# Kernel optimization log

Hardware: AMD Instinct MI355X
Metric: run time of the kernel (lower is better)

Reference implementation:

```python
import jax, jax.numpy as jnp
import numpy as np

N = 50000      # nodes
E = 400000     # edges
IN = 128       # in_dim == emb_dim (residual requires equality)
POS = 64       # pos_in_dim
EMB = 128
LN_EPS = 1e-5


def _ln(x, g, b):
    m = jnp.mean(x, axis=-1, keepdims=True)
    v = jnp.mean((x - m) ** 2, axis=-1, keepdims=True)
    return (x - m) / jnp.sqrt(v + LN_EPS) * g + b


def _gin(x, src, dst, eps, W1, b1, g1, be1, W2, b2):
    # GINConv: mlp((1+eps)*x + sum_{j in N(i)} x_j)
    agg = jax.ops.segment_sum(x[src], dst, num_segments=x.shape[0])
    h = (1.0 + eps) * x + agg
    h = jax.nn.relu(_ln(h @ W1 + b1, g1, be1))
    return h @ W2 + b2


def setup_inputs() -> dict:
    key = jax.random.key(0)
    ks = jax.random.split(key, 8)
    x = jax.random.normal(ks[0], (N, IN), jnp.float32)
    pos = jax.random.normal(ks[1], (N, POS), jnp.float32)
    edge_index = jax.random.randint(ks[2], (2, E), 0, N)
    d = IN + POS
    f32 = jnp.float32
    W1 = (jax.random.normal(ks[3], (d, EMB), f32) / np.sqrt(d))
    W2 = (jax.random.normal(ks[4], (EMB, EMB), f32) / np.sqrt(EMB))
    W1p = (jax.random.normal(ks[5], (POS, EMB), f32) / np.sqrt(POS))
    W2p = (jax.random.normal(ks[6], (EMB, EMB), f32) / np.sqrt(EMB))
    z = jnp.zeros((EMB,), f32)
    o = jnp.ones((EMB,), f32)
    return {
        "x": x, "pos": pos, "edge_index": edge_index,
        "eps": jnp.zeros((), f32), "W1": W1, "b1": z, "g1": o, "be1": z,
        "W2": W2, "b2": z, "ln_g": o, "ln_b": z,
        "epsp": jnp.zeros((), f32), "W1p": W1p, "b1p": z, "g1p": o, "be1p": z,
        "W2p": W2p, "b2p": z, "lnp_g": o, "lnp_b": z,
    }


def reference(x, pos, edge_index, eps, W1, b1, g1, be1, W2, b2, ln_g, ln_b,
              epsp, W1p, b1p, g1p, be1p, W2p, b2p, lnp_g, lnp_b):
    src, dst = edge_index[0], edge_index[1]
    node_feats = jnp.concatenate([x, pos], axis=-1)  # [N, IN+POS]
    h = jax.nn.relu(_ln(_gin(node_feats, src, dst, eps, W1, b1, g1, be1, W2, b2), ln_g, ln_b))
    p = jax.nn.relu(_ln(_gin(pos, src, dst, epsp, W1p, b1p, g1p, be1p, W2p, b2p), lnp_g, lnp_b))
    # dropout is identity in eval mode (model_drop_ratio applied only when training)
    h = h + x  # add_residual=True
    return (h, p)
```

## Files before the change

kernel.cpp:

```cpp
#include <hip/hip_runtime.h>

#define NN    50000
#define NPAD  50048
#define HB    391
#define EE    400000
#define IND   128
#define POSD  64
#define DD    192
#define EMBD  128
#define LNEPS 1e-5f
#define CAP   32

#define PREP_B 4692
#define FILL_B 1563
#define WC_B   256

typedef __attribute__((ext_vector_type(8))) short bf16x8;
typedef __attribute__((ext_vector_type(4))) unsigned short u16x4;
typedef __attribute__((ext_vector_type(4))) float f32x4;
typedef unsigned short ushort_t;
typedef unsigned int uint_t;

#define MFMA16 __builtin_amdgcn_mfma_f32_16x16x32_bf16

__device__ inline ushort_t f2bf(float f) {
  union { float f; unsigned u; } v; v.f = f;
  unsigned r = (v.u + 0x7FFFu + ((v.u >> 16) & 1u)) >> 16;
  return (ushort_t)r;
}
__device__ inline float bf2f(unsigned u) {
  union { unsigned u; float f; } v; v.u = u << 16;
  return v.f;
}

__global__ __launch_bounds__(256) void prep_k(
    const float* __restrict__ x, const float* __restrict__ pos,
    const int* __restrict__ ei,
    const float* __restrict__ W1, const float* __restrict__ W2,
    const float* __restrict__ W1p, const float* __restrict__ W2p,
    int* __restrict__ cnt, int* __restrict__ csr,
    ushort_t* __restrict__ cat, ushort_t* __restrict__ wt) {
  const int bid = blockIdx.x;
  if (bid < PREP_B) {
    int id  = bid * 256 + threadIdx.x;
    int n   = id / 24, sub = id - n * 24;
    bf16x8 o = (bf16x8){0, 0, 0, 0, 0, 0, 0, 0};
    if (n < NN) {
      const float* src = (sub < 16) ? (x + (size_t)n * IND + sub * 8)
                                    : (pos + (size_t)n * POSD + (sub - 16) * 8);
      f32x4 v0 = *(const f32x4*)(src);
      f32x4 v1 = *(const f32x4*)(src + 4);
#pragma unroll
      for (int i = 0; i < 4; ++i) {
        o[i]     = (short)f2bf(v0[i]);
        o[i + 4] = (short)f2bf(v1[i]);
      }
    }
    *(bf16x8*)(cat + (size_t)n * DD + sub * 8) = o;
  } else if (bid < PREP_B + FILL_B) {
    int e = (bid - PREP_B) * 256 + threadIdx.x;
    if (e < EE) {
      int src = ei[e];
      int dst = ei[EE + e];
      int idx = atomicAdd(&cnt[dst], 1);
      if (idx < CAP) csr[(size_t)dst * CAP + idx] = src;
    }
  } else {
    int t = (bid - PREP_B - FILL_B) * 256 + threadIdx.x;
    if (t < 24576) {
      int c = t / 192, k = t % 192;
      wt[t] = f2bf(W1[k * EMBD + c]);
    } else if (t < 40960) {
      int q = t - 24576; int c = q / 128, k = q % 128;
      wt[t] = f2bf(W2[k * EMBD + c]);
    } else if (t < 49152) {
      int q = t - 40960; int c = q / 64, k = q % 64;
      wt[t] = f2bf(W1p[k * EMBD + c]);
    } else {
      int q = t - 49152; int c = q / 128, k = q % 128;
      wt[t] = f2bf(W2p[k * EMBD + c]);
    }
  }
}

__global__ __launch_bounds__(256) void fill_k(
    const int* __restrict__ ei, int* __restrict__ cnt, int* __restrict__ csr) {
  int e = blockIdx.x * 256 + threadIdx.x;
  if (e >= EE) return;
  int src = ei[e];
  int dst = ei[EE + e];
  int idx = atomicAdd(&cnt[dst], 1);
  if (idx < CAP) csr[(size_t)dst * CAP + idx] = src;
}

__global__ __launch_bounds__(256) void wconv_k(
    const float* __restrict__ W1, const float* __restrict__ W2,
    const float* __restrict__ W1p, const float* __restrict__ W2p,
    ushort_t* __restrict__ wt) {
  int tid = blockIdx.x * 256 + threadIdx.x;
  if (tid < 24576) {
    int c = tid / 192, k = tid % 192;
    wt[tid] = f2bf(W1[k * EMBD + c]);
  } else if (tid < 40960) {
    int t = tid - 24576; int c = t / 128, k = t % 128;
    wt[tid] = f2bf(W2[k * EMBD + c]);
  } else if (tid < 49152) {
    int t = tid - 40960; int c = t / 64, k = t % 64;
    wt[tid] = f2bf(W1p[k * EMBD + c]);
  } else {
    int t = tid - 49152; int c = t / 128, k = t % 128;
    wt[tid] = f2bf(W2p[k * EMBD + c]);
  }
}

__global__ __launch_bounds__(256) void gather_k(
    const float* __restrict__ x, const float* __restrict__ pos,
    const int* __restrict__ cnt, const int* __restrict__ csr,
    const float* __restrict__ epsv, const float* __restrict__ epspv,
    ushort_t* __restrict__ h0, ushort_t* __restrict__ p0) {
  const int lane = threadIdx.x & 63;
  const int wv   = threadIdx.x >> 6;
  const int n    = blockIdx.x * 4 + wv;
  if (n >= NPAD) return;

  float a0 = 0.f, a1 = 0.f, a2 = 0.f;
  float xs0 = 0.f, xs1 = 0.f, ps = 0.f;

  if (n < NN) {
    int deg = cnt[n]; if (deg > CAP) deg = CAP;
    const int* row = csr + (size_t)n * CAP;
    int idx = (lane < deg) ? row[lane] : 0;
    int t = 0;
    for (; t + 2 <= deg; t += 2) {
      int s1 = __shfl(idx, t);
      int s2 = __shfl(idx, t + 1);
      float u0 = x[(size_t)s1 * IND + lane];
      float u1 = x[(size_t)s1 * IND + 64 + lane];
      float u2 = pos[(size_t)s1 * POSD + lane];
      float v0 = x[(size_t)s2 * IND + lane];
      float v1 = x[(size_t)s2 * IND + 64 + lane];
      float v2 = pos[(size_t)s2 * POSD + lane];
      a0 += u0 + v0; a1 += u1 + v1; a2 += u2 + v2;
    }
    if (t < deg) {
      int s1 = __shfl(idx, t);
      a0 += x[(size_t)s1 * IND + lane];
      a1 += x[(size_t)s1 * IND + 64 + lane];
      a2 += pos[(size_t)s1 * POSD + lane];
    }
    xs0 = x[(size_t)n * IND + lane];
    xs1 = x[(size_t)n * IND + 64 + lane];
    ps  = pos[(size_t)n * POSD + lane];
  }

  float e1  = 1.0f + epsv[0];
  float ep1 = 1.0f + epspv[0];
  h0[(size_t)n * DD + lane]       = f2bf(fmaf(e1, xs0, a0));
  h0[(size_t)n * DD + 64 + lane]  = f2bf(fmaf(e1, xs1, a1));
  h0[(size_t)n * DD + 128 + lane] = f2bf(fmaf(e1, ps,  a2));
  p0[(size_t)n * POSD + lane]     = f2bf(fmaf(ep1, ps, a2));
}

__global__ __launch_bounds__(256) void gather2_k(
    const ushort_t* __restrict__ cat, const int* __restrict__ cnt,
    const int* __restrict__ csr,
    const float* __restrict__ epsv, const float* __restrict__ epspv,
    ushort_t* __restrict__ h0, ushort_t* __restrict__ p0) {
  const int lane = threadIdx.x & 63;
  const int wv   = threadIdx.x >> 6;
  const int half = lane >> 5;
  const int l2   = lane & 31;
  const int n    = blockIdx.x * 8 + wv * 2 + half;

  int deg = 0;
  if (n < NN) { deg = cnt[n]; if (deg > CAP) deg = CAP; }
  int idx = (l2 < deg) ? csr[(size_t)n * CAP + l2] : 0;

  float a0 = 0.f, a1 = 0.f, a2 = 0.f, a3 = 0.f, a4 = 0.f, a5 = 0.f;
  int t = 0;
  for (; t + 2 <= deg; t += 2) {
    int s1 = __shfl(idx, half * 32 + t);
    int s2 = __shfl(idx, half * 32 + t + 1);
    const ushort_t* r1 = cat + (size_t)s1 * DD;
    const ushort_t* r2 = cat + (size_t)s2 * DD;
    u16x4 u1 = *(const u16x4*)(r1 + l2 * 4);
    uint_t v1 = *(const uint_t*)(r1 + 128 + l2 * 2);
    u16x4 u2 = *(const u16x4*)(r2 + l2 * 4);
    uint_t v2 = *(const uint_t*)(r2 + 128 + l2 * 2);
    a0 += bf2f(u1[0]) + bf2f(u2[0]);
    a1 += bf2f(u1[1]) + bf2f(u2[1]);
    a2 += bf2f(u1[2]) + bf2f(u2[2]);
    a3 += bf2f(u1[3]) + bf2f(u2[3]);
    a4 += bf2f(v1 & 0xffffu) + bf2f(v2 & 0xffffu);
    a5 += bf2f(v1 >> 16) + bf2f(v2 >> 16);
  }
  if (t < deg) {
    int s1 = __shfl(idx, half * 32 + t);
    const ushort_t* r1 = cat + (size_t)s1 * DD;
    u16x4 u1 = *(const u16x4*)(r1 + l2 * 4);
    uint_t v1 = *(const uint_t*)(r1 + 128 + l2 * 2);
    a0 += bf2f(u1[0]); a1 += bf2f(u1[1]);
    a2 += bf2f(u1[2]); a3 += bf2f(u1[3]);
    a4 += bf2f(v1 & 0xffffu); a5 += bf2f(v1 >> 16);
  }

  const float e1  = 1.0f + epsv[0];
  const float ep1 = 1.0f + epspv[0];
  const ushort_t* self = cat + (size_t)n * DD;
  u16x4 su = *(const u16x4*)(self + l2 * 4);
  uint_t sv = *(const uint_t*)(self + 128 + l2 * 2);

  u16x4 o;
  o[0] = f2bf(fmaf(e1, bf2f(su[0]), a0));
  o[1] = f2bf(fmaf(e1, bf2f(su[1]), a1));
  o[2] = f2bf(fmaf(e1, bf2f(su[2]), a2));
  o[3] = f2bf(fmaf(e1, bf2f(su[3]), a3));
  *(u16x4*)(h0 + (size_t)n * DD + l2 * 4) = o;

  float p4 = bf2f(sv & 0xffffu), p5 = bf2f(sv >> 16);
  uint_t oh = (uint_t)f2bf(fmaf(e1, p4, a4)) |
              ((uint_t)f2bf(fmaf(e1, p5, a5)) << 16);
  *(uint_t*)(h0 + (size_t)n * DD + 128 + l2 * 2) = oh;
  uint_t op = (uint_t)f2bf(fmaf(ep1, p4, a4)) |
              ((uint_t)f2bf(fmaf(ep1, p5, a5)) << 16);
  *(uint_t*)(p0 + (size_t)n * POSD + l2 * 2) = op;
}

__device__ inline void ln_epi(f32x4 (&acc)[2][8],
                              const float* __restrict__ bias,
                              const float* __restrict__ gam,
                              const float* __restrict__ bet, int c0) {
  float bv[8], gv[8], bev[8];
#pragma unroll
  for (int nt = 0; nt < 8; ++nt) {
    bv[nt]  = bias[nt * 16 + c0];
    gv[nt]  = gam[nt * 16 + c0];
    bev[nt] = bet[nt * 16 + c0];
  }
#pragma unroll
  for (int mt = 0; mt < 2; ++mt) {
#pragma unroll
    for (int r = 0; r < 4; ++r) {
      float s = 0.f, sq = 0.f;
#pragma unroll
      for (int nt = 0; nt < 8; ++nt) {
        float v = acc[mt][nt][r] + bv[nt];
        acc[mt][nt][r] = v;
        s += v; sq += v * v;
      }
#pragma unroll
      for (int off = 1; off < 16; off <<= 1) {
        s  += __shfl_xor(s, off);
        sq += __shfl_xor(sq, off);
      }
      float mean = s * (1.0f / 128.0f);
      float var  = sq * (1.0f / 128.0f) - mean * mean;
      float rstd = rsqrtf(var + LNEPS);
#pragma unroll
      for (int nt = 0; nt < 8; ++nt) {
        acc[mt][nt][r] =
            fmaxf(fmaf((acc[mt][nt][r] - mean) * rstd, gv[nt], bev[nt]), 0.f);
      }
    }
  }
}

__device__ inline void act_write(char* act, f32x4 (&acc)[2][8], int g, int c0) {
#pragma unroll
  for (int mt = 0; mt < 2; ++mt)
#pragma unroll
    for (int nt = 0; nt < 8; ++nt)
#pragma unroll
      for (int r = 0; r < 4; ++r) {
        int lr   = mt * 16 + g * 4 + r;
        int byte = lr * 256 + (((nt * 16 + c0) * 2) ^ ((lr & 7) << 4));
        *(ushort_t*)(act + byte) = f2bf(acc[mt][nt][r]);
      }
}

__device__ inline void stage_w(const ushort_t* __restrict__ src, char* dst,
                               int rowbytes, int chunks, int tid) {
  int cpr = rowbytes >> 4;
  for (int i = tid; i < chunks; i += 256) {
    int row  = i / cpr;
    int colb = (i - row * cpr) << 4;
    *(bf16x8*)(dst + row * rowbytes + (colb ^ ((row & 7) << 4))) =
        *(const bf16x8*)(src + (size_t)i * 8);
  }
}

__global__ __launch_bounds__(256) void mlp_k(
    const ushort_t* __restrict__ h0, const ushort_t* __restrict__ p0,
    const ushort_t* __restrict__ wt,
    const float* __restrict__ b1, const float* __restrict__ g1,
    const float* __restrict__ be1,
    const float* __restrict__ b2, const float* __restrict__ lng,
    const float* __restrict__ lnb,
    const float* __restrict__ b1p, const float* __restrict__ g1p,
    const float* __restrict__ be1p,
    const float* __restrict__ b2p, const float* __restrict__ lnpg,
    const float* __restrict__ lnpb,
    const float* __restrict__ x, float* __restrict__ out) {
  __shared__ __align__(16) char smem[81920];
  const int tid  = threadIdx.x;
  const int lane = tid & 63;
  const int wv   = tid >> 6;
  const int g    = lane >> 4;
  const int c0   = lane & 15;
  const int bid  = blockIdx.x;
  char* act = smem + 49152 + wv * 8192;

  f32x4 acc[2][8];

  if (bid < HB) {
    const int m0 = bid * 128;
    stage_w(wt, smem, 384, 3072, tid);
    bf16x8 a0[6], a1[6];
    const size_t r0 = (size_t)(m0 + wv * 32 + c0) * DD;
    const size_t r1 = r0 + (size_t)16 * DD;
#pragma unroll
    for (int ks = 0; ks < 6; ++ks) {
      a0[ks] = *(const bf16x8*)(h0 + r0 + ks * 32 + g * 8);
      a1[ks] = *(const bf16x8*)(h0 + r1 + ks * 32 + g * 8);
    }
    __syncthreads();

#pragma unroll
    for (int mt = 0; mt < 2; ++mt)
#pragma unroll
      for (int nt = 0; nt < 8; ++nt) acc[mt][nt] = (f32x4){0.f, 0.f, 0.f, 0.f};
#pragma unroll
    for (int ks = 0; ks < 6; ++ks)
#pragma unroll
      for (int nt = 0; nt < 8; ++nt) {
        int wrow = nt * 16 + c0;
        bf16x8 b = *(const bf16x8*)(smem + wrow * 384 +
                                    ((ks * 64 + g * 16) ^ ((wrow & 7) << 4)));
        acc[0][nt] = MFMA16(a0[ks], b, acc[0][nt], 0, 0, 0);
        acc[1][nt] = MFMA16(a1[ks], b, acc[1][nt], 0, 0, 0);
      }
    ln_epi(acc, b1, g1, be1, c0);
    act_write(act, acc, g, c0);
    __syncthreads();
    stage_w(wt + 24576, smem, 256, 2048, tid);
    __syncthreads();

#pragma unroll
    for (int mt = 0; mt < 2; ++mt)
#pragma unroll
      for (int nt = 0; nt < 8; ++nt) acc[mt][nt] = (f32x4){0.f, 0.f, 0.f, 0.f};
#pragma unroll
    for (int ks = 0; ks < 4; ++ks) {
      bf16x8 am[2];
#pragma unroll
      for (int mt = 0; mt < 2; ++mt) {
        int lr = mt * 16 + c0;
        am[mt] = *(const bf16x8*)(act + lr * 256 +
                                  (((ks * 32 + g * 8) * 2) ^ ((lr & 7) << 4)));
      }
#pragma unroll
      for (int nt = 0; nt < 8; ++nt) {
        int wrow = nt * 16 + c0;
        bf16x8 b = *(const bf16x8*)(smem + wrow * 256 +
                                    ((ks * 64 + g * 16) ^ ((wrow & 7) << 4)));
        acc[0][nt] = MFMA16(am[0], b, acc[0][nt], 0, 0, 0);
        acc[1][nt] = MFMA16(am[1], b, acc[1][nt], 0, 0, 0);
      }
    }
    ln_epi(acc, b2, lng, lnb, c0);
#pragma unroll
    for (int mt = 0; mt < 2; ++mt)
#pragma unroll
      for (int nt = 0; nt < 8; ++nt)
#pragma unroll
        for (int r = 0; r < 4; ++r) {
          int node = m0 + wv * 32 + mt * 16 + g * 4 + r;
          int col  = nt * 16 + c0;
          if (node < NN)
            out[(size_t)node * EMBD + col] =
                acc[mt][nt][r] + x[(size_t)node * IND + col];
        }
  } else {
    const int m0 = (bid - HB) * 128;
    stage_w(wt + 40960, smem, 128, 1024, tid);
    stage_w(wt + 49152, smem + 16384, 256, 2048, tid);
    bf16x8 a0[2], a1[2];
    const size_t r0 = (size_t)(m0 + wv * 32 + c0) * POSD;
    const size_t r1 = r0 + (size_t)16 * POSD;
#pragma unroll
    for (int ks = 0; ks < 2; ++ks) {
      a0[ks] = *(const bf16x8*)(p0 + r0 + ks * 32 + g * 8);
      a1[ks] = *(const bf16x8*)(p0 + r1 + ks * 32 + g * 8);
    }
    __syncthreads();

#pragma unroll
    for (int mt = 0; mt < 2; ++mt)
#pragma unroll
      for (int nt = 0; nt < 8; ++nt) acc[mt][nt] = (f32x4){0.f, 0.f, 0.f, 0.f};
#pragma unroll
    for (int ks = 0; ks < 2; ++ks)
#pragma unroll
      for (int nt = 0; nt < 8; ++nt) {
        int wrow = nt * 16 + c0;
        bf16x8 b = *(const bf16x8*)(smem + wrow * 128 +
                                    ((ks * 64 + g * 16) ^ ((wrow & 7) << 4)));
        acc[0][nt] = MFMA16(a0[ks], b, acc[0][nt], 0, 0, 0);
        acc[1][nt] = MFMA16(a1[ks], b, acc[1][nt], 0, 0, 0);
      }
    ln_epi(acc, b1p, g1p, be1p, c0);
    act_write(act, acc, g, c0);

#pragma unroll
    for (int mt = 0; mt < 2; ++mt)
#pragma unroll
      for (int nt = 0; nt < 8; ++nt) acc[mt][nt] = (f32x4){0.f, 0.f, 0.f, 0.f};
#pragma unroll
    for (int ks = 0; ks < 4; ++ks) {
      bf16x8 am[2];
#pragma unroll
      for (int mt = 0; mt < 2; ++mt) {
        int lr = mt * 16 + c0;
        am[mt] = *(const bf16x8*)(act + lr * 256 +
                                  (((ks * 32 + g * 8) * 2) ^ ((lr & 7) << 4)));
      }
#pragma unroll
      for (int nt = 0; nt < 8; ++nt) {
        int wrow = nt * 16 + c0;
        bf16x8 b = *(const bf16x8*)(smem + 16384 + wrow * 256 +
                                    ((ks * 64 + g * 16) ^ ((wrow & 7) << 4)));
        acc[0][nt] = MFMA16(am[0], b, acc[0][nt], 0, 0, 0);
        acc[1][nt] = MFMA16(am[1], b, acc[1][nt], 0, 0, 0);
      }
    }
    ln_epi(acc, b2p, lnpg, lnpb, c0);
#pragma unroll
    for (int mt = 0; mt < 2; ++mt)
#pragma unroll
      for (int nt = 0; nt < 8; ++nt)
#pragma unroll
        for (int r = 0; r < 4; ++r) {
          int node = m0 + wv * 32 + mt * 16 + g * 4 + r;
          int col  = nt * 16 + c0;
          if (node < NN)
            out[(size_t)NN * EMBD + (size_t)node * EMBD + col] = acc[mt][nt][r];
        }
  }
}

extern "C" void kernel_launch(void* const* d_in, const int* in_sizes, int n_in,
                              void* d_out, int out_size, void* d_ws, size_t ws_size,
                              hipStream_t stream) {
  const float* x    = (const float*)d_in[0];
  const float* pos  = (const float*)d_in[1];
  const int*   ei   = (const int*)d_in[2];
  const float* eps  = (const float*)d_in[3];
  const float* W1   = (const float*)d_in[4];
  const float* b1   = (const float*)d_in[5];
  const float* g1   = (const float*)d_in[6];
  const float* be1  = (const float*)d_in[7];
  const float* W2   = (const float*)d_in[8];
  const float* b2   = (const float*)d_in[9];
  const float* lng  = (const float*)d_in[10];
  const float* lnb  = (const float*)d_in[11];
  const float* epsp = (const float*)d_in[12];
  const float* W1p  = (const float*)d_in[13];
  const float* b1p  = (const float*)d_in[14];
  const float* g1p  = (const float*)d_in[15];
  const float* be1p = (const float*)d_in[16];
  const float* W2p  = (const float*)d_in[17];
  const float* b2p  = (const float*)d_in[18];
  const float* lnpg = (const float*)d_in[19];
  const float* lnpb = (const float*)d_in[20];

  char* ws = (char*)d_ws;
  float* out = (float*)d_out;

  const size_t CATB = (size_t)NPAD * DD * 2;
  const size_t P0B  = (size_t)NPAD * POSD * 2;
  const size_t NEED_BIG = 200000 + 6400000 + CATB + CATB + P0B + 131072;

  int* cnt = (int*)ws;
  int* csr = (int*)(ws + 200000);

  hipMemsetAsync(cnt, 0, (size_t)NN * sizeof(int), stream);

  if (ws_size >= NEED_BIG) {
    ushort_t* cat = (ushort_t*)(ws + 6600000);
    ushort_t* h0  = (ushort_t*)(ws + 6600000 + CATB);
    ushort_t* p0  = (ushort_t*)(ws + 6600000 + 2 * CATB);
    ushort_t* wt  = (ushort_t*)(ws + 6600000 + 2 * CATB + P0B);

    prep_k<<<PREP_B + FILL_B + WC_B, 256, 0, stream>>>(
        x, pos, ei, W1, W2, W1p, W2p, cnt, csr, cat, wt);
    gather2_k<<<NPAD / 8, 256, 0, stream>>>(cat, cnt, csr, eps, epsp, h0, p0);
    mlp_k<<<2 * HB, 256, 0, stream>>>(
        h0, p0, wt, b1, g1, be1, b2, lng, lnb,
        b1p, g1p, be1p, b2p, lnpg, lnpb, x, out);
  } else {
    ushort_t* h0 = (ushort_t*)(ws + 6600000);
    ushort_t* p0 = (ushort_t*)(ws + 6600000 + CATB);
    ushort_t* wt = (ushort_t*)(ws + 6600000 + CATB + P0B);

    fill_k<<<(EE + 255) / 256, 256, 0, stream>>>(ei, cnt, csr);
    wconv_k<<<256, 256, 0, stream>>>(W1, W2, W1p, W2p, wt);
    gather_k<<<NPAD / 4, 256, 0, stream>>>(x, pos, cnt, csr, eps, epsp, h0, p0);
    mlp_k<<<2 * HB, 256, 0, stream>>>(
        h0, p0, wt, b1, g1, be1, b2, lng, lnb,
        b1p, g1p, be1p, b2p, lnpg, lnpb, x, out);
  }
}
```

Before: 116.6 us.

## Transpose MFMA operands so accumulators hold row-contiguous features; unroll gather by 4

The MLP kernel swaps the MFMA A/B operands (weights as A, activations as B), so each lane's accumulator holds 4 consecutive feature columns of one node. This lets the LayerNorm reduction use two cross-lane shuffles instead of four per row, and lets bias, gamma, beta, residual loads and output stores use 16-byte vectors instead of scalar strided accesses. The activation LDS write becomes 8-byte vector stores. Separately, the bf16 gather loop is unrolled to four neighbors per iteration to put more loads in flight.

```diff
diff --git a/kernel.cpp b/kernel.cpp
--- a/kernel.cpp
+++ b/kernel.cpp
@@ -134,13 +134,9 @@
     for (; t + 2 <= deg; t += 2) {
       int s1 = __shfl(idx, t);
       int s2 = __shfl(idx, t + 1);
-      float u0 = x[(size_t)s1 * IND + lane];
-      float u1 = x[(size_t)s1 * IND + 64 + lane];
-      float u2 = pos[(size_t)s1 * POSD + lane];
-      float v0 = x[(size_t)s2 * IND + lane];
-      float v1 = x[(size_t)s2 * IND + 64 + lane];
-      float v2 = pos[(size_t)s2 * POSD + lane];
-      a0 += u0 + v0; a1 += u1 + v1; a2 += u2 + v2;
+      a0 += x[(size_t)s1 * IND + lane] + x[(size_t)s2 * IND + lane];
+      a1 += x[(size_t)s1 * IND + 64 + lane] + x[(size_t)s2 * IND + 64 + lane];
+      a2 += pos[(size_t)s1 * POSD + lane] + pos[(size_t)s2 * POSD + lane];
     }
     if (t < deg) {
       int s1 = __shfl(idx, t);
@@ -178,23 +174,32 @@
 
   float a0 = 0.f, a1 = 0.f, a2 = 0.f, a3 = 0.f, a4 = 0.f, a5 = 0.f;
   int t = 0;
-  for (; t + 2 <= deg; t += 2) {
+  for (; t + 4 <= deg; t += 4) {
     int s1 = __shfl(idx, half * 32 + t);
     int s2 = __shfl(idx, half * 32 + t + 1);
+    int s3 = __shfl(idx, half * 32 + t + 2);
+    int s4 = __shfl(idx, half * 32 + t + 3);
     const ushort_t* r1 = cat + (size_t)s1 * DD;
     const ushort_t* r2 = cat + (size_t)s2 * DD;
+    const ushort_t* r3 = cat + (size_t)s3 * DD;
+    const ushort_t* r4 = cat + (size_t)s4 * DD;
     u16x4 u1 = *(const u16x4*)(r1 + l2 * 4);
+    u16x4 u2 = *(const u16x4*)(r2 + l2 * 4);
+    u16x4 u3 = *(const u16x4*)(r3 + l2 * 4);
+    u16x4 u4 = *(const u16x4*)(r4 + l2 * 4);
     uint_t v1 = *(const uint_t*)(r1 + 128 + l2 * 2);
-    u16x4 u2 = *(const u16x4*)(r2 + l2 * 4);
     uint_t v2 = *(const uint_t*)(r2 + 128 + l2 * 2);
-    a0 += bf2f(u1[0]) + bf2f(u2[0]);
-    a1 += bf2f(u1[1]) + bf2f(u2[1]);
-    a2 += bf2f(u1[2]) + bf2f(u2[2]);
-    a3 += bf2f(u1[3]) + bf2f(u2[3]);
-    a4 += bf2f(v1 & 0xffffu) + bf2f(v2 & 0xffffu);
-    a5 += bf2f(v1 >> 16) + bf2f(v2 >> 16);
-  }
-  if (t < deg) {
+    uint_t v3 = *(const uint_t*)(r3 + 128 + l2 * 2);
+    uint_t v4 = *(const uint_t*)(r4 + 128 + l2 * 2);
+    a0 += (bf2f(u1[0]) + bf2f(u2[0])) + (bf2f(u3[0]) + bf2f(u4[0]));
+    a1 += (bf2f(u1[1]) + bf2f(u2[1])) + (bf2f(u3[1]) + bf2f(u4[1]));
+    a2 += (bf2f(u1[2]) + bf2f(u2[2])) + (bf2f(u3[2]) + bf2f(u4[2]));
+    a3 += (bf2f(u1[3]) + bf2f(u2[3])) + (bf2f(u3[3]) + bf2f(u4[3]));
+    a4 += (bf2f(v1 & 0xffffu) + bf2f(v2 & 0xffffu)) +
+          (bf2f(v3 & 0xffffu) + bf2f(v4 & 0xffffu));
+    a5 += (bf2f(v1 >> 16) + bf2f(v2 >> 16)) + (bf2f(v3 >> 16) + bf2f(v4 >> 16));
+  }
+  for (; t < deg; ++t) {
     int s1 = __shfl(idx, half * 32 + t);
     const ushort_t* r1 = cat + (size_t)s1 * DD;
     u16x4 u1 = *(const u16x4*)(r1 + l2 * 4);
@@ -226,56 +231,55 @@
   *(uint_t*)(p0 + (size_t)n * POSD + l2 * 2) = op;
 }
 
-__device__ inline void ln_epi(f32x4 (&acc)[2][8],
-                              const float* __restrict__ bias,
-                              const float* __restrict__ gam,
-                              const float* __restrict__ bet, int c0) {
-  float bv[8], gv[8], bev[8];
+__device__ inline void ln_epi_T(f32x4 (&acc)[8][2],
+                                const float* __restrict__ bias,
+                                const float* __restrict__ gam,
+                                const float* __restrict__ bet, int g) {
+  f32x4 bv[8], gv[8], bev[8];
 #pragma unroll
   for (int nt = 0; nt < 8; ++nt) {
-    bv[nt]  = bias[nt * 16 + c0];
-    gv[nt]  = gam[nt * 16 + c0];
-    bev[nt] = bet[nt * 16 + c0];
+    bv[nt]  = *(const f32x4*)(bias + nt * 16 + g * 4);
+    gv[nt]  = *(const f32x4*)(gam  + nt * 16 + g * 4);
+    bev[nt] = *(const f32x4*)(bet  + nt * 16 + g * 4);
   }
 #pragma unroll
   for (int mt = 0; mt < 2; ++mt) {
-#pragma unroll
-    for (int r = 0; r < 4; ++r) {
-      float s = 0.f, sq = 0.f;
-#pragma unroll
-      for (int nt = 0; nt < 8; ++nt) {
-        float v = acc[mt][nt][r] + bv[nt];
-        acc[mt][nt][r] = v;
+    float s = 0.f, sq = 0.f;
+#pragma unroll
+    for (int nt = 0; nt < 8; ++nt)
+#pragma unroll
+      for (int r = 0; r < 4; ++r) {
+        float v = acc[nt][mt][r] + bv[nt][r];
+        acc[nt][mt][r] = v;
         s += v; sq += v * v;
       }
-#pragma unroll
-      for (int off = 1; off < 16; off <<= 1) {
-        s  += __shfl_xor(s, off);
-        sq += __shfl_xor(sq, off);
-      }
-      float mean = s * (1.0f / 128.0f);
-      float var  = sq * (1.0f / 128.0f) - mean * mean;
-      float rstd = rsqrtf(var + LNEPS);
-#pragma unroll
-      for (int nt = 0; nt < 8; ++nt) {
-        acc[mt][nt][r] =
-            fmaxf(fmaf((acc[mt][nt][r] - mean) * rstd, gv[nt], bev[nt]), 0.f);
-      }
-    }
-  }
-}
-
-__device__ inline void act_write(char* act, f32x4 (&acc)[2][8], int g, int c0) {
-#pragma unroll
-  for (int mt = 0; mt < 2; ++mt)
+    s  += __shfl_xor(s, 16);  sq += __shfl_xor(sq, 16);
+    s  += __shfl_xor(s, 32);  sq += __shfl_xor(sq, 32);
+    float mean = s * (1.0f / 128.0f);
+    float var  = sq * (1.0f / 128.0f) - mean * mean;
+    float rstd = rsqrtf(var + LNEPS);
 #pragma unroll
     for (int nt = 0; nt < 8; ++nt)
 #pragma unroll
-      for (int r = 0; r < 4; ++r) {
-        int lr   = mt * 16 + g * 4 + r;
-        int byte = lr * 256 + (((nt * 16 + c0) * 2) ^ ((lr & 7) << 4));
-        *(ushort_t*)(act + byte) = f2bf(acc[mt][nt][r]);
-      }
+      for (int r = 0; r < 4; ++r)
+        acc[nt][mt][r] = fmaxf(
+            fmaf((acc[nt][mt][r] - mean) * rstd, gv[nt][r], bev[nt][r]), 0.f);
+  }
+}
+
+__device__ inline void act_write_T(char* act, f32x4 (&acc)[8][2], int g, int c0) {
+#pragma unroll
+  for (int mt = 0; mt < 2; ++mt) {
+    int lr = mt * 16 + c0;
+    int sw = (lr & 7) << 4;
+#pragma unroll
+    for (int nt = 0; nt < 8; ++nt) {
+      u16x4 o;
+#pragma unroll
+      for (int r = 0; r < 4; ++r) o[r] = f2bf(acc[nt][mt][r]);
+      *(u16x4*)(act + lr * 256 + ((nt * 32 + g * 8) ^ sw)) = o;
+    }
+  }
 }
 
 __device__ inline void stage_w(const ushort_t* __restrict__ src, char* dst,
@@ -310,7 +314,7 @@
   const int bid  = blockIdx.x;
   char* act = smem + 49152 + wv * 8192;
 
-  f32x4 acc[2][8];
+  f32x4 acc[8][2];
 
   if (bid < HB) {
     const int m0 = bid * 128;
@@ -326,29 +330,29 @@
     __syncthreads();
 
 #pragma unroll
-    for (int mt = 0; mt < 2; ++mt)
-#pragma unroll
-      for (int nt = 0; nt < 8; ++nt) acc[mt][nt] = (f32x4){0.f, 0.f, 0.f, 0.f};
+    for (int nt = 0; nt < 8; ++nt)
+#pragma unroll
+      for (int mt = 0; mt < 2; ++mt) acc[nt][mt] = (f32x4){0.f, 0.f, 0.f, 0.f};
 #pragma unroll
     for (int ks = 0; ks < 6; ++ks)
 #pragma unroll
       for (int nt = 0; nt < 8; ++nt) {
         int wrow = nt * 16 + c0;
-        bf16x8 b = *(const bf16x8*)(smem + wrow * 384 +
+        bf16x8 w = *(const bf16x8*)(smem + wrow * 384 +
                                     ((ks * 64 + g * 16) ^ ((wrow & 7) << 4)));
-        acc[0][nt] = MFMA16(a0[ks], b, acc[0][nt], 0, 0, 0);
-        acc[1][nt] = MFMA16(a1[ks], b, acc[1][nt], 0, 0, 0);
-      }
-    ln_epi(acc, b1, g1, be1, c0);
-    act_write(act, acc, g, c0);
+        acc[nt][0] = MFMA16(w, a0[ks], acc[nt][0], 0, 0, 0);
+        acc[nt][1] = MFMA16(w, a1[ks], acc[nt][1], 0, 0, 0);
+      }
+    ln_epi_T(acc, b1, g1, be1, g);
+    act_write_T(act, acc, g, c0);
     __syncthreads();
     stage_w(wt + 24576, smem, 256, 2048, tid);
     __syncthreads();
 
 #pragma unroll
-    for (int mt = 0; mt < 2; ++mt)
-#pragma unroll
-      for (int nt = 0; nt < 8; ++nt) acc[mt][nt] = (f32x4){0.f, 0.f, 0.f, 0.f};
+    for (int nt = 0; nt < 8; ++nt)
+#pragma unroll
+      for (int mt = 0; mt < 2; ++mt) acc[nt][mt] = (f32x4){0.f, 0.f, 0.f, 0.f};
 #pragma unroll
     for (int ks = 0; ks < 4; ++ks) {
       bf16x8 am[2];
@@ -356,30 +360,33 @@
       for (int mt = 0; mt < 2; ++mt) {
         int lr = mt * 16 + c0;
         am[mt] = *(const bf16x8*)(act + lr * 256 +
-                                  (((ks * 32 + g * 8) * 2) ^ ((lr & 7) << 4)));
+                                  ((ks * 64 + g * 16) ^ ((lr & 7) << 4)));
       }
 #pragma unroll
       for (int nt = 0; nt < 8; ++nt) {
         int wrow = nt * 16 + c0;
-        bf16x8 b = *(const bf16x8*)(smem + wrow * 256 +
+        bf16x8 w = *(const bf16x8*)(smem + wrow * 256 +
                                     ((ks * 64 + g * 16) ^ ((wrow & 7) << 4)));
-        acc[0][nt] = MFMA16(am[0], b, acc[0][nt], 0, 0, 0);
-        acc[1][nt] = MFMA16(am[1], b, acc[1][nt], 0, 0, 0);
-      }
-    }
-    ln_epi(acc, b2, lng, lnb, c0);
-#pragma unroll
-    for (int mt = 0; mt < 2; ++mt)
-#pragma unroll
-      for (int nt = 0; nt < 8; ++nt)
-#pragma unroll
-        for (int r = 0; r < 4; ++r) {
-          int node = m0 + wv * 32 + mt * 16 + g * 4 + r;
-          int col  = nt * 16 + c0;
-          if (node < NN)
-            out[(size_t)node * EMBD + col] =
-                acc[mt][nt][r] + x[(size_t)node * IND + col];
+        acc[nt][0] = MFMA16(w, am[0], acc[nt][0], 0, 0, 0);
+        acc[nt][1] = MFMA16(w, am[1], acc[nt][1], 0, 0, 0);
+      }
+    }
+    ln_epi_T(acc, b2, lng, lnb, g);
+#pragma unroll
+    for (int mt = 0; mt < 2; ++mt) {
+      int node = m0 + wv * 32 + mt * 16 + c0;
+      if (node < NN) {
+#pragma unroll
+        for (int nt = 0; nt < 8; ++nt) {
+          int f0 = nt * 16 + g * 4;
+          f32x4 xr = *(const f32x4*)(x + (size_t)node * IND + f0);
+          f32x4 o;
+#pragma unroll
+          for (int r = 0; r < 4; ++r) o[r] = acc[nt][mt][r] + xr[r];
+          *(f32x4*)(out + (size_t)node * EMBD + f0) = o;
         }
+      }
+    }
   } else {
     const int m0 = (bid - HB) * 128;
     stage_w(wt + 40960, smem, 128, 1024, tid);
@@ -395,26 +402,26 @@
     __syncthreads();
 
 #pragma unroll
-    for (int mt = 0; mt < 2; ++mt)
-#pragma unroll
-      for (int nt = 0; nt < 8; ++nt) acc[mt][nt] = (f32x4){0.f, 0.f, 0.f, 0.f};
+    for (int nt = 0; nt < 8; ++nt)
+#pragma unroll
+      for (int mt = 0; mt < 2; ++mt) acc[nt][mt] = (f32x4){0.f, 0.f, 0.f, 0.f};
 #pragma unroll
     for (int ks = 0; ks < 2; ++ks)
 #pragma unroll
       for (int nt = 0; nt < 8; ++nt) {
         int wrow = nt * 16 + c0;
-        bf16x8 b = *(const bf16x8*)(smem + wrow * 128 +
+        bf16x8 w = *(const bf16x8*)(smem + wrow * 128 +
                                     ((ks * 64 + g * 16) ^ ((wrow & 7) << 4)));
-        acc[0][nt] = MFMA16(a0[ks], b, acc[0][nt], 0, 0, 0);
-        acc[1][nt] = MFMA16(a1[ks], b, acc[1][nt], 0, 0, 0);
-      }
-    ln_epi(acc, b1p, g1p, be1p, c0);
-    act_write(act, acc, g, c0);
-
-#pragma unroll
-    for (int mt = 0; mt < 2; ++mt)
-#pragma unroll
-      for (int nt = 0; nt < 8; ++nt) acc[mt][nt] = (f32x4){0.f, 0.f, 0.f, 0.f};
+        acc[nt][0] = MFMA16(w, a0[ks], acc[nt][0], 0, 0, 0);
+        acc[nt][1] = MFMA16(w, a1[ks], acc[nt][1], 0, 0, 0);
+      }
+    ln_epi_T(acc, b1p, g1p, be1p, g);
+    act_write_T(act, acc, g, c0);
+
+#pragma unroll
+    for (int nt = 0; nt < 8; ++nt)
+#pragma unroll
+      for (int mt = 0; mt < 2; ++mt) acc[nt][mt] = (f32x4){0.f, 0.f, 0.f, 0.f};
 #pragma unroll
     for (int ks = 0; ks < 4; ++ks) {
       bf16x8 am[2];
@@ -422,29 +429,32 @@
       for (int mt = 0; mt < 2; ++mt) {
         int lr = mt * 16 + c0;
         am[mt] = *(const bf16x8*)(act + lr * 256 +
-                                  (((ks * 32 + g * 8) * 2) ^ ((lr & 7) << 4)));
+                                  ((ks * 64 + g * 16) ^ ((lr & 7) << 4)));
       }
 #pragma unroll
       for (int nt = 0; nt < 8; ++nt) {
         int wrow = nt * 16 + c0;
-        bf16x8 b = *(const bf16x8*)(smem + 16384 + wrow * 256 +
+        bf16x8 w = *(const bf16x8*)(smem + 16384 + wrow * 256 +
                                     ((ks * 64 + g * 16) ^ ((wrow & 7) << 4)));
-        acc[0][nt] = MFMA16(am[0], b, acc[0][nt], 0, 0, 0);
-        acc[1][nt] = MFMA16(am[1], b, acc[1][nt], 0, 0, 0);
-      }
-    }
-    ln_epi(acc, b2p, lnpg, lnpb, c0);
-#pragma unroll
-    for (int mt = 0; mt < 2; ++mt)
-#pragma unroll
-      for (int nt = 0; nt < 8; ++nt)
-#pragma unroll
-        for (int r = 0; r < 4; ++r) {
-          int node = m0 + wv * 32 + mt * 16 + g * 4 + r;
-          int col  = nt * 16 + c0;
-          if (node < NN)
-            out[(size_t)NN * EMBD + (size_t)node * EMBD + col] = acc[mt][nt][r];
+        acc[nt][0] = MFMA16(w, am[0], acc[nt][0], 0, 0, 0);
+        acc[nt][1] = MFMA16(w, am[1], acc[nt][1], 0, 0, 0);
+      }
+    }
+    ln_epi_T(acc, b2p, lnpg, lnpb, g);
+#pragma unroll
+    for (int mt = 0; mt < 2; ++mt) {
+      int node = m0 + wv * 32 + mt * 16 + c0;
+      if (node < NN) {
+#pragma unroll
+        for (int nt = 0; nt < 8; ++nt) {
+          int f0 = nt * 16 + g * 4;
+          f32x4 o;
+#pragma unroll
+          for (int r = 0; r < 4; ++r) o[r] = acc[nt][mt][r];
+          *(f32x4*)(out + (size_t)NN * EMBD + (size_t)node * EMBD + f0) = o;
         }
+      }
+    }
   }
 }
 
```

Result: no change. 114.8 us (-1.6%).
